# Kernel optimization log

Measured on AMD Instinct MI355X. Metric: run time of the kernel, lower is better.

## Reference

```python
import jax, jax.numpy as jnp
import numpy as np

N = 10000
E = 160000
NT = 4      # num_types
NB = 8      # bessel basis size
U = 32      # env_embed_multiplicity
R_MAX = 6.0
AVG_NEIGH = 16.0
POLY_P = 6.0


def _mlp(x, Ws):
    # nequip ScalarMLPFunction: no biases, forward-normalized weights, SiLU between layers
    n = len(Ws)
    for i, W in enumerate(Ws):
        x = x @ (W * (1.0 / jnp.sqrt(jnp.float32(W.shape[0]))))
        if i < n - 1:
            x = jax.nn.silu(x)
    return x


def _poly_cutoff(r, rc, p=POLY_P):
    x = r / rc
    out = (1.0 - ((p + 1.0) * (p + 2.0) / 2.0) * x ** p
           + p * (p + 2.0) * x ** (p + 1.0)
           - (p * (p + 1.0) / 2.0) * x ** (p + 2.0))
    return out * (x < 1.0)


def _weighted_channels(edge_attr, w):
    # MakeWeightedChannels: per-edge, per-channel weight for each irrep block
    # edge_attr: [E,4] = (0e | 1o), w: [E,U,2] -> out [E,U,4]
    wd = jnp.concatenate([w[:, :, 0:1], jnp.repeat(w[:, :, 1:2], 3, axis=-1)], axis=-1)
    return edge_attr[:, None, :] * wd


def _forward(edge_index, node_attrs, edge_attr, edge_embed, edge_length,
             W2b0, W2b1, W2b2, Wenv0, Wlat0, Wlat1, Wenv1, Wfin0, Wfin1,
             Wlin_s, Wlin_v, resnet_params):
    n_nodes = node_attrs.shape[0]
    n_edges = edge_attr.shape[0]
    center, neigh = edge_index[0], edge_index[1]
    cut = _poly_cutoff(edge_length, R_MAX)[:, None]           # [E,1], same per-layer cutoff
    env_norm = 1.0 / jnp.sqrt(AVG_NEIGH)
    sqrt3 = jnp.sqrt(3.0)
    c = jnp.exp(resnet_params)                                 # resnet update coefficients

    # ---- two-body latent (layer 0 latent)
    lat_in = jnp.concatenate([node_attrs[center], node_attrs[neigh], edge_embed], axis=-1)
    latents = _mlp(lat_in, [W2b0, W2b1, W2b2]) * cut           # [E,512]
    norm2 = c[0] ** 2
    latents = latents * (c[0] / jnp.sqrt(norm2))

    # env-embed MLP layer 0: feature weights + env weights
    w0 = _mlp(latents, [Wenv0])                                # [E,4U]
    w_feat = w0[:, :2 * U].reshape(n_edges, U, 2)
    w_env = w0[:, 2 * U:].reshape(n_edges, U, 2)
    features = _weighted_channels(edge_attr, w_feat)           # [E,U,4]

    def env_embed_edges(w_env):
        env_w = _weighted_channels(edge_attr, w_env)           # [E,U,4]
        env = jax.ops.segment_sum(env_w, center, num_segments=n_nodes) * env_norm
        return env[center]                                     # [E,U,4]

    # ---- layer 0 TP ('uuu', e3nn component norm): (0e+1o) x (0e+1o) -> [0e,0e,1o,1o]
    env_e = env_embed_edges(w_env)
    t0 = features[:, :, 0] * env_e[:, :, 0]
    t1 = jnp.sum(features[:, :, 1:] * env_e[:, :, 1:], axis=-1) / sqrt3
    v0 = features[:, :, 0:1] * env_e[:, :, 1:]
    v1 = features[:, :, 1:] * env_e[:, :, 0:1]
    scalars = jnp.concatenate([t0, t1], axis=-1)               # [E,2U]
    # e3nn Linear mixing full_out_irreps back to (0e+1o) x U
    alpha = 1.0 / jnp.sqrt(2.0 * U)
    y_s = (scalars @ Wlin_s) * alpha                           # [E,U]
    x_v = jnp.concatenate([v0, v1], axis=1)                    # [E,2U,3]
    y_v = jnp.einsum('ekd,ko->eod', x_v, Wlin_v) * alpha       # [E,U,3]
    features = jnp.concatenate([y_s[..., None], y_v], axis=-1)

    # latent resnet update
    new_lat = _mlp(jnp.concatenate([latents, scalars], axis=-1), [Wlat0, Wlat1]) * cut
    latents = (jnp.sqrt(norm2) * latents + c[1] * new_lat) / jnp.sqrt(norm2 + c[1] ** 2)
    norm2 = norm2 + c[1] ** 2

    w_env = _mlp(latents, [Wenv1]).reshape(n_edges, U, 2)

    # ---- layer 1 TP (last layer): only scalar outputs [0e,0e]
    env_e = env_embed_edges(w_env)
    t0 = features[:, :, 0] * env_e[:, :, 0]
    t1 = jnp.sum(features[:, :, 1:] * env_e[:, :, 1:], axis=-1) / sqrt3
    scalars = jnp.concatenate([t0, t1], axis=-1)               # [E,2U]
    # (the last-layer Linear output features are never used downstream -> skipped)

    # ---- final latent
    new_lat = _mlp(jnp.concatenate([latents, scalars], axis=-1), [Wfin0, Wfin1]) * cut
    latents = (jnp.sqrt(norm2) * latents + c[2] * new_lat) / jnp.sqrt(norm2 + c[2] ** 2)
    return latents                                             # [E,512] edge features


def setup_inputs() -> dict:
    key = jax.random.key(0)
    ks = jax.random.split(key, 20)
    edge_index = jax.random.randint(ks[0], (2, E), 0, N)
    node_types = jax.random.randint(ks[1], (N,), 0, NT)
    node_attrs = jax.nn.one_hot(node_types, NT, dtype=jnp.float32)
    edge_length = jax.random.uniform(ks[2], (E,), minval=0.5, maxval=R_MAX)
    vec = jax.random.normal(ks[3], (E, 3), dtype=jnp.float32)
    unit = vec / jnp.linalg.norm(vec, axis=-1, keepdims=True)
    # component-normalized real spherical harmonics: l=0 -> 1, l=1 -> sqrt(3)*unit
    edge_attr = jnp.concatenate([jnp.ones((E, 1), jnp.float32), jnp.sqrt(3.0) * unit], axis=-1)
    nb = jnp.arange(1, NB + 1, dtype=jnp.float32)
    edge_embed = (jnp.sqrt(2.0 / R_MAX)
                  * jnp.sin(nb[None, :] * jnp.pi * edge_length[:, None] / R_MAX)
                  / edge_length[:, None])
    w = lambda k, shp: jax.random.normal(k, shp, dtype=jnp.float32)
    return {
        'edge_index': edge_index, 'node_attrs': node_attrs, 'edge_attr': edge_attr,
        'edge_embed': edge_embed, 'edge_length': edge_length,
        'W2b0': w(ks[4], (2 * NT + NB, 128)), 'W2b1': w(ks[5], (128, 256)), 'W2b2': w(ks[6], (256, 512)),
        'Wenv0': w(ks[7], (512, 4 * U)),
        'Wlat0': w(ks[8], (512 + 2 * U, 512)), 'Wlat1': w(ks[9], (512, 512)),
        'Wenv1': w(ks[10], (512, 2 * U)),
        'Wfin0': w(ks[11], (512 + 2 * U, 512)), 'Wfin1': w(ks[12], (512, 512)),
        'Wlin_s': w(ks[13], (2 * U, U)), 'Wlin_v': w(ks[14], (2 * U, U)),
        'resnet_params': jnp.zeros((3,), jnp.float32),
    }


def reference(edge_index, node_attrs, edge_attr, edge_embed, edge_length,
              W2b0, W2b1, W2b2, Wenv0, Wlat0, Wlat1, Wenv1, Wfin0, Wfin1,
              Wlin_s, Wlin_v, resnet_params):
    return _forward(edge_index, node_attrs, edge_attr, edge_embed, edge_length,
                    W2b0, W2b1, W2b2, Wenv0, Wlat0, Wlat1, Wenv1, Wfin0, Wfin1,
                    Wlin_s, Wlin_v, resnet_params)
```

## Files before the change

kernel.cpp:

```cpp
#include <hip/hip_runtime.h>
#include <math.h>

#define E_EDGES 160000
#define N_NODES 10000

typedef __attribute__((ext_vector_type(8))) __bf16 bf16x8;
typedef __attribute__((ext_vector_type(4))) float f32x4;
typedef __attribute__((ext_vector_type(4))) unsigned int u32x4;

__device__ __forceinline__ unsigned short f2bf(float x) {
    unsigned u = __float_as_uint(x);
    u += 0x7fff + ((u >> 16) & 1);
    return (unsigned short)(u >> 16);
}
__device__ __forceinline__ float bf2f(unsigned short h) {
    return __uint_as_float(((unsigned)h) << 16);
}
__device__ __forceinline__ void gload16(const unsigned short* g, unsigned short* l) {
    __builtin_amdgcn_global_load_lds(
        (const __attribute__((address_space(1))) void*)g,
        (__attribute__((address_space(3))) void*)l, 16, 0, 0);
}

__global__ __launch_bounds__(256)
void prep_kernel(const int* __restrict__ ei, const float* __restrict__ na,
                 const float* __restrict__ embed, const float* __restrict__ elen,
                 float* __restrict__ cut, unsigned short* __restrict__ A16b,
                 int* __restrict__ deg)
{
    int e = blockIdx.x * blockDim.x + threadIdx.x;
    if (e >= E_EDGES) return;
    float r  = elen[e];
    float x  = r * (1.0f / 6.0f);
    float x2 = x * x;
    float x6 = x2 * x2 * x2;
    float c = 1.0f - 28.0f * x6 + 48.0f * x6 * x - 21.0f * x6 * x2;
    cut[e] = (x < 1.0f) ? c : 0.0f;
    int ctr = ei[e];
    int ngh = ei[E_EDGES + e];
    atomicAdd(&deg[ctr], 1);
    float4 ac = *(const float4*)(na + (size_t)ctr * 4);
    float4 an = *(const float4*)(na + (size_t)ngh * 4);
    float4 b0 = *(const float4*)(embed + (size_t)e * 8);
    float4 b1 = *(const float4*)(embed + (size_t)e * 8 + 4);
    unsigned short* o = A16b + (size_t)e * 32;
    o[0]  = f2bf(ac.x); o[1]  = f2bf(ac.y); o[2]  = f2bf(ac.z); o[3]  = f2bf(ac.w);
    o[4]  = f2bf(an.x); o[5]  = f2bf(an.y); o[6]  = f2bf(an.z); o[7]  = f2bf(an.w);
    o[8]  = f2bf(b0.x); o[9]  = f2bf(b0.y); o[10] = f2bf(b0.z); o[11] = f2bf(b0.w);
    o[12] = f2bf(b1.x); o[13] = f2bf(b1.y); o[14] = f2bf(b1.z); o[15] = f2bf(b1.w);
    #pragma unroll
    for (int i = 16; i < 32; ++i) o[i] = 0;
}

__global__ __launch_bounds__(256)
void wtrans_all(const float* __restrict__ w0, const float* __restrict__ w1,
                const float* __restrict__ w2, const float* __restrict__ w3,
                const float* __restrict__ w4, const float* __restrict__ w5,
                const float* __restrict__ w6, const float* __restrict__ w7,
                const float* __restrict__ w8, unsigned short* __restrict__ wbuf)
{
    int blk = blockIdx.x;
    const float* W; int K, N, Kpad, Npad; size_t dbase; int lstart; float sc;
    const float s16  = 0.25f;
    const float s128 = 0.088388347648318447f;
    const float s256 = 0.0625f;
    const float s512 = 0.044194173824159223f;
    const float s576 = 0.041666666666666664f;
    if      (blk <   16) { W=w0; K=16;  N=128; Kpad=32;  Npad=128; dbase=0;       lstart=0;    sc=s16;  }
    else if (blk <  144) { W=w1; K=128; N=256; Kpad=128; Npad=256; dbase=4096;    lstart=16;   sc=s128; }
    else if (blk <  656) { W=w2; K=256; N=512; Kpad=256; Npad=512; dbase=36864;   lstart=144;  sc=s256; }
    else if (blk <  912) { W=w3; K=512; N=128; Kpad=512; Npad=128; dbase=167936;  lstart=656;  sc=s512; }
    else if (blk < 2064) { W=w4; K=576; N=512; Kpad=576; Npad=512; dbase=233472;  lstart=912;  sc=s576; }
    else if (blk < 3088) { W=w5; K=512; N=512; Kpad=512; Npad=512; dbase=528384;  lstart=2064; sc=s512; }
    else if (blk < 3344) { W=w6; K=512; N=64;  Kpad=512; Npad=128; dbase=790528;  lstart=3088; sc=s512; }
    else if (blk < 4496) { W=w7; K=576; N=512; Kpad=576; Npad=512; dbase=856064;  lstart=3344; sc=s576; }
    else                 { W=w8; K=512; N=512; Kpad=512; Npad=512; dbase=1150976; lstart=4496; sc=s512; }
    int local = (blk - lstart) * 256 + threadIdx.x;
    int n = local % Npad, k = local / Npad;
    if (k >= Kpad) return;
    float v = (k < K && n < N) ? W[(size_t)k * N + n] * sc : 0.0f;
    wbuf[dbase + (size_t)n * Kpad + k] = f2bf(v);
}

__global__ __launch_bounds__(1024)
void scan_kernel(const int* __restrict__ deg, int* __restrict__ offs)
{
    __shared__ int part[1024];
    int t = threadIdx.x;
    int base = t * 10;
    int loc[10];
    int s = 0;
    #pragma unroll
    for (int i = 0; i < 10; ++i) {
        int idx = base + i;
        int d = (idx < N_NODES) ? deg[idx] : 0;
        loc[i] = s; s += d;
    }
    part[t] = s;
    __syncthreads();
    for (int o = 1; o < 1024; o <<= 1) {
        int v = (t >= o) ? part[t - o] : 0;
        __syncthreads();
        part[t] += v;
        __syncthreads();
    }
    int excl = (t > 0) ? part[t - 1] : 0;
    #pragma unroll
    for (int i = 0; i < 10; ++i) {
        int idx = base + i;
        if (idx < N_NODES) offs[idx] = excl + loc[i];
    }
    if (t == 1023) offs[N_NODES] = part[1023];
}

__global__ __launch_bounds__(256)
void fill_kernel(const int* __restrict__ ei, const int* __restrict__ offs,
                 int* __restrict__ cnt, int* __restrict__ elist)
{
    int e = blockIdx.x * blockDim.x + threadIdx.x;
    if (e >= E_EDGES) return;
    int c = ei[e];
    int pos = offs[c] + atomicAdd(&cnt[c], 1);
    elist[pos] = e;
}

__global__ __launch_bounds__(256)
void sortseg_kernel(const int* __restrict__ offs, int* __restrict__ elist)
{
    int node = blockIdx.x * 4 + (threadIdx.x >> 6);
    int l = threadIdx.x & 63;
    if (node >= N_NODES) return;
    int b = offs[node], en = offs[node + 1];
    int deg = en - b;
    if (deg <= 1) return;
    if (deg <= 64) {
        int v = (l < deg) ? elist[b + l] : 0x7fffffff;
        #pragma unroll
        for (int k = 2; k <= 64; k <<= 1) {
            #pragma unroll
            for (int j = k >> 1; j > 0; j >>= 1) {
                int o = __shfl_xor(v, j);
                bool dirUp = ((l & k) == 0);
                bool lower = ((l & j) == 0);
                int mn = v < o ? v : o;
                int mx = v < o ? o : v;
                v = (dirUp == lower) ? mn : mx;
            }
        }
        if (l < deg) elist[b + l] = v;
    } else if (l == 0) {
        for (int i = b + 1; i < en; ++i) {
            int v = elist[i];
            int j = i - 1;
            while (j >= b && elist[j] > v) { elist[j + 1] = elist[j]; --j; }
            elist[j + 1] = v;
        }
    }
}

__global__ __launch_bounds__(256)
void envgather_kernel(const unsigned short* __restrict__ Wb, int wstride, int woff,
                      const float* __restrict__ ea, const int* __restrict__ offs,
                      const int* __restrict__ elist, float* __restrict__ env)
{
    int n = blockIdx.x * 2 + (threadIdx.x >> 7);
    int t = threadIdx.x & 127;
    if (n >= N_NODES) return;
    int u = t >> 2, comp = t & 3;
    int widx = woff + u * 2 + (comp ? 1 : 0);
    int beg = offs[n], end = offs[n + 1];
    float acc = 0.0f;
    for (int i = beg; i < end; ++i) {
        int e = elist[i];
        float w = bf2f(Wb[(size_t)e * wstride + widx]);
        float a = ea[(size_t)e * 4 + comp];
        acc += a * w;
    }
    env[(size_t)n * 128 + t] = acc * 0.25f;
}

template<int EPIL, bool CONCAT>
__global__ __launch_bounds__(256)
void gemm_bf16(const unsigned short* __restrict__ A1, const unsigned short* __restrict__ A2,
               int KA1, int K, const unsigned short* __restrict__ Bt,
               int nx, int ldc, int Nstore,
               float* __restrict__ Cf, unsigned short* __restrict__ Cb,
               const float* __restrict__ cut, const float* __restrict__ rp)
{
    __shared__ __align__(16) unsigned short SB[3][2][128 * 32];
    const int tid  = threadIdx.x;
    const int lane = tid & 63;
    const int wid  = tid >> 6;
    const int wr   = wid >> 1, wc = wid & 1;
    const int nwg = gridDim.x;
    const int fid = blockIdx.x;
    const int q = nwg >> 3, r = nwg & 7;
    const int xcd = fid & 7, j = fid >> 3;
    const int L = ((xcd < r) ? xcd * (q + 1) : r * (q + 1) + (xcd - r) * q) + j;
    const int bn = (L % nx) * 128;
    const int bm = (L / nx) * 128;

    const int l15 = lane & 15;
    const int l4r = lane >> 2;
    const int sk8 = (((lane & 3) ^ ((lane >> 3) & 3)) << 3);
    const int rk8 = ((((lane >> 4) ^ ((l15 >> 1) & 3)) & 3) << 3);
    const int KA2 = K - KA1;
    const int T   = K >> 5;

    f32x4 acc[4][4] = {};

    auto stage = [&](int t, int b) {
        int k0 = t << 5;
        #pragma unroll
        for (int i = 0; i < 2; ++i) {
            int ch  = (wid << 1) + i;
            int row = (ch << 4) + l4r;
            const unsigned short* gp;
            if (!CONCAT || k0 < KA1)
                gp = A1 + (size_t)(bm + row) * KA1 + k0 + sk8;
            else
                gp = A2 + (size_t)(bm + row) * KA2 + (k0 - KA1) + sk8;
            gload16(gp, &SB[b][0][ch << 9]);
            const unsigned short* gpb = Bt + (size_t)(bn + row) * K + k0 + sk8;
            gload16(gpb, &SB[b][1][ch << 9]);
        }
    };

    stage(0, 0);
    if (T >= 2) stage(1, 1);

    for (int t = 0; t < T; ++t) {
        if (t < T - 1) asm volatile("s_waitcnt vmcnt(4)" ::: "memory");
        else           asm volatile("s_waitcnt vmcnt(0)" ::: "memory");
        __builtin_amdgcn_s_barrier();
        __builtin_amdgcn_sched_barrier(0);

        if (t + 2 < T) stage(t + 2, (t + 2) % 3);

        const unsigned short* As = &SB[t % 3][0][0];
        const unsigned short* Bs = &SB[t % 3][1][0];
        bf16x8 af[4], bfr[4];
        #pragma unroll
        for (int m = 0; m < 4; ++m)
            af[m] = __builtin_bit_cast(bf16x8, *(const u32x4*)&As[(wr * 64 + m * 16 + l15) * 32 + rk8]);
        #pragma unroll
        for (int n = 0; n < 4; ++n)
            bfr[n] = __builtin_bit_cast(bf16x8, *(const u32x4*)&Bs[(wc * 64 + n * 16 + l15) * 32 + rk8]);

        __builtin_amdgcn_s_setprio(1);
        #pragma unroll
        for (int m = 0; m < 4; ++m)
            #pragma unroll
            for (int n = 0; n < 4; ++n)
                acc[m][n] = __builtin_amdgcn_mfma_f32_16x16x32_bf16(af[m], bfr[n], acc[m][n], 0, 0, 0);
        __builtin_amdgcn_s_setprio(0);

        asm volatile("s_waitcnt lgkmcnt(0)" ::: "memory");
        __builtin_amdgcn_sched_barrier(0);
    }

    #pragma unroll
    for (int m = 0; m < 4; ++m) {
        int rbase = bm + wr * 64 + m * 16 + ((lane >> 4) << 2);
        #pragma unroll
        for (int n = 0; n < 4; ++n) {
            int col = bn + wc * 64 + n * 16 + l15;
            if (col < Nstore) {
                #pragma unroll
                for (int rr = 0; rr < 4; ++rr) {
                    int row = rbase + rr;
                    float v = acc[m][n][rr];
                    size_t off2 = (size_t)row * ldc + col;
                    if (EPIL == 0) {
                        Cb[off2] = f2bf(v);
                    } else if (EPIL == 1) {
                        v = v / (1.0f + __expf(-v));
                        Cb[off2] = f2bf(v);
                    } else if (EPIL == 2) {
                        v *= cut[row];
                        Cb[off2] = f2bf(v);
                    }
                }
            }
        }
    }
}

template<int EPIL2>
__global__ __launch_bounds__(512)
void fused_mlp(const unsigned short* __restrict__ A1,
               const unsigned short* __restrict__ A2,
               const unsigned short* __restrict__ W1t,
               const unsigned short* __restrict__ W2t,
               float* __restrict__ Cf, unsigned short* __restrict__ Cb,
               const float* __restrict__ cut, const float* __restrict__ rp)
{
    __shared__ __align__(16) unsigned short Hl[128 * 512];
    __shared__ __align__(16) unsigned short SA[3][128 * 32];
    const int tid  = threadIdx.x;
    const int lane = tid & 63;
    const int wid  = tid >> 6;
    const int l15  = lane & 15;
    const int l4r  = lane >> 2;
    const int lk8  = (lane >> 4) << 3;
    const int sk8  = (((lane & 3) ^ ((lane >> 3) & 3)) << 3);
    const int rk8  = ((((lane >> 4) ^ ((l15 >> 1) & 3)) & 3) << 3);
    const int bm   = blockIdx.x * 128;
    const int hcol0 = wid * 64;
    const int ocol0 = wid * 64;

    auto stage = [&](int t, int b) {
        int k0 = t << 5;
        int row = (wid << 4) + l4r;
        const unsigned short* gp;
        if (k0 < 512) gp = A1 + (size_t)(bm + row) * 512 + k0 + sk8;
        else          gp = A2 + (size_t)(bm + row) * 64 + (k0 - 512) + sk8;
        gload16(gp, &SA[b][wid << 9]);
    };

    f32x4 acc1[8][4] = {};
    stage(0, 0);
    stage(1, 1);

    for (int t = 0; t < 18; ++t) {
        __builtin_amdgcn_sched_barrier(0);
        if (t < 17) asm volatile("s_waitcnt vmcnt(1)" ::: "memory");
        else        asm volatile("s_waitcnt vmcnt(0)" ::: "memory");
        __builtin_amdgcn_s_barrier();
        __builtin_amdgcn_sched_barrier(0);

        const unsigned short* As = &SA[t % 3][0];
        int k0 = t << 5;
        bf16x8 af[8], wf[4];
        #pragma unroll
        for (int mi = 0; mi < 8; ++mi)
            af[mi] = __builtin_bit_cast(bf16x8, *(const u32x4*)&As[(mi * 16 + l15) * 32 + rk8]);
        #pragma unroll
        for (int ni = 0; ni < 4; ++ni) {
            int hc = hcol0 + ni * 16 + l15;
            wf[ni] = __builtin_bit_cast(bf16x8, *(const u32x4*)(W1t + (size_t)hc * 576 + k0 + lk8));
        }
        __builtin_amdgcn_sched_barrier(0);
        if (t + 2 < 18) stage(t + 2, (t + 2) % 3);
        __builtin_amdgcn_sched_barrier(0);
        asm volatile("s_waitcnt lgkmcnt(0)" ::: "memory");
        __builtin_amdgcn_sched_barrier(0);

        __builtin_amdgcn_s_setprio(1);
        #pragma unroll
        for (int mi = 0; mi < 8; ++mi)
            #pragma unroll
            for (int ni = 0; ni < 4; ++ni)
                acc1[mi][ni] = __builtin_amdgcn_mfma_f32_16x16x32_bf16(af[mi], wf[ni], acc1[mi][ni], 0, 0, 0);
        __builtin_amdgcn_s_setprio(0);
    }

    #pragma unroll
    for (int mi = 0; mi < 8; ++mi)
        #pragma unroll
        for (int ni = 0; ni < 4; ++ni)
            #pragma unroll
            for (int rr = 0; rr < 4; ++rr) {
                int er = mi * 16 + ((lane >> 4) << 2) + rr;
                int hc = hcol0 + ni * 16 + l15;
                float v = acc1[mi][ni][rr];
                v = v / (1.0f + __expf(-v));
                int slotp = (hc >> 3) ^ (er & 7);
                Hl[er * 512 + slotp * 8 + (hc & 7)] = f2bf(v);
            }
    asm volatile("s_waitcnt lgkmcnt(0)" ::: "memory");
    __builtin_amdgcn_s_barrier();
    __builtin_amdgcn_sched_barrier(0);

    f32x4 acc2[8][4] = {};
    #pragma unroll 1
    for (int kt = 0; kt < 16; ++kt) {
        bf16x8 hf[8], w2f[4];
        #pragma unroll
        for (int fa = 0; fa < 8; ++fa) {
            int er = fa * 16 + l15;
            int slotp = (kt * 4 + (lane >> 4)) ^ (er & 7);
            hf[fa] = __builtin_bit_cast(bf16x8, *(const u32x4*)&Hl[er * 512 + slotp * 8]);
        }
        #pragma unroll
        for (int fb = 0; fb < 4; ++fb) {
            int oc = ocol0 + fb * 16 + l15;
            w2f[fb] = __builtin_bit_cast(bf16x8, *(const u32x4*)(W2t + (size_t)oc * 512 + kt * 32 + lk8));
        }
        __builtin_amdgcn_s_setprio(1);
        #pragma unroll
        for (int fa = 0; fa < 8; ++fa)
            #pragma unroll
            for (int fb = 0; fb < 4; ++fb)
                acc2[fa][fb] = __builtin_amdgcn_mfma_f32_16x16x32_bf16(hf[fa], w2f[fb], acc2[fa][fb], 0, 0, 0);
        __builtin_amdgcn_s_setprio(0);
    }

    float c0 = __expf(rp[0]), c1 = __expf(rp[1]), c2 = __expf(rp[2]);
    #pragma unroll
    for (int fa = 0; fa < 8; ++fa) {
        int rbase = bm + fa * 16 + ((lane >> 4) << 2);
        #pragma unroll
        for (int fb = 0; fb < 4; ++fb) {
            int col = ocol0 + fb * 16 + l15;
            #pragma unroll
            for (int rr = 0; rr < 4; ++rr) {
                int row = rbase + rr;
                float v = acc2[fa][fb][rr];
                size_t off2 = (size_t)row * 512 + col;
                if (EPIL2 == 3) {
                    float old = bf2f(Cb[off2]);
                    v = (c0 * old + c1 * v * cut[row]) * rsqrtf(c0 * c0 + c1 * c1);
                    Cb[off2] = f2bf(v);
                } else {
                    float old = bf2f(Cb[off2]);
                    float n2 = c0 * c0 + c1 * c1;
                    v = (sqrtf(n2) * old + c2 * v * cut[row]) * rsqrtf(n2 + c2 * c2);
                    Cf[off2] = v;
                }
            }
        }
    }
}

__global__ __launch_bounds__(256)
void tp0_kernel(const unsigned short* __restrict__ W0b, const float* __restrict__ ea,
                const float* __restrict__ env, const int* __restrict__ ei,
                const float* __restrict__ Ws, const float* __restrict__ Wv,
                unsigned short* __restrict__ scalb, unsigned short* __restrict__ feat2b)
{
    __shared__ float sc[8][64];
    __shared__ float xv[8][64][3];
    __shared__ float Wsl[2048];
    __shared__ float Wvl[2048];
    int tid = threadIdx.x;
    const float alpha = 0.125f;
    #pragma unroll
    for (int i = 0; i < 8; ++i) {
        Wsl[tid + i * 256] = Ws[tid + i * 256] * alpha;
        Wvl[tid + i * 256] = Wv[tid + i * 256] * alpha;
    }
    int le = tid >> 5;
    int u  = tid & 31;
    int e  = blockIdx.x * 8 + le;
    int c  = ei[e];
    float4 a = *(const float4*)(ea + (size_t)e * 4);
    const float* ep = env + (size_t)c * 128 + u * 4;
    float e0 = ep[0], e1 = ep[1], e2 = ep[2], e3 = ep[3];
    float wf0 = bf2f(W0b[(size_t)e * 128 + u * 2]);
    float wf1 = bf2f(W0b[(size_t)e * 128 + u * 2 + 1]);
    float f0 = a.x * wf0;
    float f1 = a.y * wf1, f2 = a.z * wf1, f3 = a.w * wf1;
    const float rs3 = 0.57735026918962576f;
    float t0 = f0 * e0;
    float t1 = (f1 * e1 + f2 * e2 + f3 * e3) * rs3;
    scalb[(size_t)e * 64 + u]      = f2bf(t0);
    scalb[(size_t)e * 64 + 32 + u] = f2bf(t1);
    sc[le][u]      = t0;
    sc[le][32 + u] = t1;
    xv[le][u][0] = f0 * e1; xv[le][u][1] = f0 * e2; xv[le][u][2] = f0 * e3;
    xv[le][32 + u][0] = f1 * e0; xv[le][32 + u][1] = f2 * e0; xv[le][32 + u][2] = f3 * e0;
    __syncthreads();
    float ys = 0.0f, yv0 = 0.0f, yv1 = 0.0f, yv2 = 0.0f;
    #pragma unroll 8
    for (int k = 0; k < 64; ++k) {
        float ws = Wsl[k * 32 + u];
        float wv = Wvl[k * 32 + u];
        ys  = fmaf(sc[le][k], ws, ys);
        yv0 = fmaf(xv[le][k][0], wv, yv0);
        yv1 = fmaf(xv[le][k][1], wv, yv1);
        yv2 = fmaf(xv[le][k][2], wv, yv2);
    }
    ushort4 ov;
    ov.x = f2bf(ys);
    ov.y = f2bf(yv0);
    ov.z = f2bf(yv1);
    ov.w = f2bf(yv2);
    *(ushort4*)(feat2b + (size_t)e * 128 + u * 4) = ov;
}

__global__ __launch_bounds__(256)
void tp1_kernel(const unsigned short* __restrict__ feat2b, const float* __restrict__ env,
                const int* __restrict__ ei, unsigned short* __restrict__ scalb)
{
    int idx = blockIdx.x * blockDim.x + threadIdx.x;
    if (idx >= E_EDGES * 32) return;
    int e = idx >> 5, u = idx & 31;
    int c = ei[e];
    const float* ep = env + (size_t)c * 128 + u * 4;
    ushort4 f4 = *(const ushort4*)(feat2b + (size_t)e * 128 + u * 4);
    float fx = bf2f(f4.x), fy = bf2f(f4.y), fz = bf2f(f4.z), fw = bf2f(f4.w);
    const float rs3 = 0.57735026918962576f;
    float t0 = fx * ep[0];
    float t1 = (fy * ep[1] + fz * ep[2] + fw * ep[3]) * rs3;
    scalb[(size_t)e * 64 + u]      = f2bf(t0);
    scalb[(size_t)e * 64 + 32 + u] = f2bf(t1);
}

extern "C" void kernel_launch(void* const* d_in, const int* in_sizes, int n_in,
                              void* d_out, int out_size, void* d_ws, size_t ws_size,
                              hipStream_t stream)
{
    const int*   ei     = (const int*)d_in[0];
    const float* na     = (const float*)d_in[1];
    const float* ea     = (const float*)d_in[2];
    const float* embed  = (const float*)d_in[3];
    const float* elen   = (const float*)d_in[4];
    const float* W2b0   = (const float*)d_in[5];
    const float* W2b1   = (const float*)d_in[6];
    const float* W2b2   = (const float*)d_in[7];
    const float* Wenv0  = (const float*)d_in[8];
    const float* Wlat0  = (const float*)d_in[9];
    const float* Wlat1  = (const float*)d_in[10];
    const float* Wenv1  = (const float*)d_in[11];
    const float* Wfin0  = (const float*)d_in[12];
    const float* Wfin1  = (const float*)d_in[13];
    const float* Wlin_s = (const float*)d_in[14];
    const float* Wlin_v = (const float*)d_in[15];
    const float* rp     = (const float*)d_in[16];

    float* L = (float*)d_out;
    const size_t E = E_EDGES;

    char* ws = (char*)d_ws;
    size_t off = 0;
    auto alloc = [&](size_t b) { void* p = ws + off; off += (b + 255) & ~(size_t)255; return p; };
    float*          cutb   = (float*)alloc(E * 4);
    unsigned short* wbuf   = (unsigned short*)alloc((size_t)1413120 * 2);
    float*          envb   = (float*)alloc((size_t)N_NODES * 128 * 4);
    unsigned short* scalb  = (unsigned short*)alloc(E * 64 * 2);
    unsigned short* feat2b = (unsigned short*)alloc(E * 128 * 2);
    unsigned short* Lb     = (unsigned short*)alloc(E * 512 * 2);
    int*            degcnt = (int*)alloc((size_t)2 * N_NODES * 4);
    int*            offs   = (int*)alloc((N_NODES + 1) * 4);
    int*            elist  = (int*)alloc(E * 4);
    unsigned short* A16b   = (unsigned short*)alloc(E * 32 * 2);
    unsigned short* H1b    = (unsigned short*)alloc(E * 128 * 2);
    unsigned short* H2b    = (unsigned short*)alloc(E * 256 * 2);
    unsigned short* R1b    = (unsigned short*)alloc(E * 128 * 2);
    unsigned short* WE1b   = (unsigned short*)alloc(E * 64 * 2);
    int* deg = degcnt;
    int* cnt = degcnt + N_NODES;

    unsigned short* W2b0t  = wbuf;
    unsigned short* W2b1t  = wbuf + 4096;
    unsigned short* W2b2t  = wbuf + 36864;
    unsigned short* Wenv0t = wbuf + 167936;
    unsigned short* Wlat0t = wbuf + 233472;
    unsigned short* Wlat1t = wbuf + 528384;
    unsigned short* Wenv1t = wbuf + 790528;
    unsigned short* Wfin0t = wbuf + 856064;
    unsigned short* Wfin1t = wbuf + 1150976;
    wtrans_all<<<5520, 256, 0, stream>>>(W2b0, W2b1, W2b2, Wenv0, Wlat0, Wlat1,
                                         Wenv1, Wfin0, Wfin1, wbuf);

    hipMemsetAsync(degcnt, 0, (size_t)2 * N_NODES * 4, stream);
    prep_kernel<<<E_EDGES / 256, 256, 0, stream>>>(ei, na, embed, elen, cutb, A16b, deg);
    scan_kernel<<<1, 1024, 0, stream>>>(deg, offs);
    fill_kernel<<<E_EDGES / 256, 256, 0, stream>>>(ei, offs, cnt, elist);
    sortseg_kernel<<<N_NODES / 4, 256, 0, stream>>>(offs, elist);

    gemm_bf16<1, false><<<1250, 256, 0, stream>>>(A16b, nullptr, 32, 32, W2b0t, 1, 128, 128, nullptr, H1b, nullptr, nullptr);
    gemm_bf16<1, false><<<2500, 256, 0, stream>>>(H1b, nullptr, 128, 128, W2b1t, 2, 256, 256, nullptr, H2b, nullptr, nullptr);
    gemm_bf16<2, false><<<5000, 256, 0, stream>>>(H2b, nullptr, 256, 256, W2b2t, 4, 512, 512, nullptr, Lb, cutb, nullptr);

    gemm_bf16<0, false><<<1250, 256, 0, stream>>>(Lb, nullptr, 512, 512, Wenv0t, 1, 128, 128, nullptr, R1b, nullptr, nullptr);

    envgather_kernel<<<N_NODES / 2, 256, 0, stream>>>(R1b, 128, 64, ea, offs, elist, envb);
    tp0_kernel<<<E_EDGES / 8, 256, 0, stream>>>(R1b, ea, envb, ei, Wlin_s, Wlin_v, scalb, feat2b);

    fused_mlp<3><<<1250, 512, 0, stream>>>(Lb, scalb, Wlat0t, Wlat1t, nullptr, Lb, cutb, rp);

    gemm_bf16<0, false><<<1250, 256, 0, stream>>>(Lb, nullptr, 512, 512, Wenv1t, 1, 64, 64, nullptr, WE1b, nullptr, nullptr);

    envgather_kernel<<<N_NODES / 2, 256, 0, stream>>>(WE1b, 64, 0, ea, offs, elist, envb);
    tp1_kernel<<<E_EDGES * 32 / 256, 256, 0, stream>>>(feat2b, envb, ei, scalb);

    fused_mlp<4><<<1250, 512, 0, stream>>>(Lb, scalb, Wfin0t, Wfin1t, L, Lb, cutb, rp);
}
```

Measured before the change: 1.183 ms.

## Fuse two-body MLP into one kernel and halve fused_mlp row tile

Replaces the three separate two-body MLP GEMMs with a single mlp2b kernel that keeps the hidden activations (128 and 256 wide) in LDS per 64-edge tile, removing the global write and read of the H1/H2 intermediates. The fused_mlp kernels also drop from 128-row to 64-row tiles, halving LDS use and accumulator registers and doubling the grid, which should allow more resident blocks. The cost is that weights are re-read per smaller tile, and the mlp2b weight fragments are loaded directly from global memory without staging.

```diff
diff --git a/kernel.cpp b/kernel.cpp
--- a/kernel.cpp
+++ b/kernel.cpp
@@ -15,6 +15,9 @@
 }
 __device__ __forceinline__ float bf2f(unsigned short h) {
     return __uint_as_float(((unsigned)h) << 16);
+}
+__device__ __forceinline__ float siluf(float v) {
+    return v / (1.0f + __expf(-v));
 }
 __device__ __forceinline__ void gload16(const unsigned short* g, unsigned short* l) {
     __builtin_amdgcn_global_load_lds(
@@ -179,13 +182,12 @@
     env[(size_t)n * 128 + t] = acc * 0.25f;
 }
 
-template<int EPIL, bool CONCAT>
-__global__ __launch_bounds__(256)
-void gemm_bf16(const unsigned short* __restrict__ A1, const unsigned short* __restrict__ A2,
-               int KA1, int K, const unsigned short* __restrict__ Bt,
+template<int EPIL>
+__global__ __launch_bounds__(256)
+void gemm_bf16(const unsigned short* __restrict__ A1,
+               int K, const unsigned short* __restrict__ Bt,
                int nx, int ldc, int Nstore,
-               float* __restrict__ Cf, unsigned short* __restrict__ Cb,
-               const float* __restrict__ cut, const float* __restrict__ rp)
+               unsigned short* __restrict__ Cb)
 {
     __shared__ __align__(16) unsigned short SB[3][2][128 * 32];
     const int tid  = threadIdx.x;
@@ -204,7 +206,6 @@
     const int l4r = lane >> 2;
     const int sk8 = (((lane & 3) ^ ((lane >> 3) & 3)) << 3);
     const int rk8 = ((((lane >> 4) ^ ((l15 >> 1) & 3)) & 3) << 3);
-    const int KA2 = K - KA1;
     const int T   = K >> 5;
 
     f32x4 acc[4][4] = {};
@@ -215,14 +216,8 @@
         for (int i = 0; i < 2; ++i) {
             int ch  = (wid << 1) + i;
             int row = (ch << 4) + l4r;
-            const unsigned short* gp;
-            if (!CONCAT || k0 < KA1)
-                gp = A1 + (size_t)(bm + row) * KA1 + k0 + sk8;
-            else
-                gp = A2 + (size_t)(bm + row) * KA2 + (k0 - KA1) + sk8;
-            gload16(gp, &SB[b][0][ch << 9]);
-            const unsigned short* gpb = Bt + (size_t)(bn + row) * K + k0 + sk8;
-            gload16(gpb, &SB[b][1][ch << 9]);
+            gload16(A1 + (size_t)(bm + row) * K + k0 + sk8, &SB[b][0][ch << 9]);
+            gload16(Bt + (size_t)(bn + row) * K + k0 + sk8, &SB[b][1][ch << 9]);
         }
     };
 
@@ -269,18 +264,133 @@
                 #pragma unroll
                 for (int rr = 0; rr < 4; ++rr) {
                     int row = rbase + rr;
-                    float v = acc[m][n][rr];
-                    size_t off2 = (size_t)row * ldc + col;
-                    if (EPIL == 0) {
-                        Cb[off2] = f2bf(v);
-                    } else if (EPIL == 1) {
-                        v = v / (1.0f + __expf(-v));
-                        Cb[off2] = f2bf(v);
-                    } else if (EPIL == 2) {
-                        v *= cut[row];
-                        Cb[off2] = f2bf(v);
-                    }
+                    Cb[(size_t)row * ldc + col] = f2bf(acc[m][n][rr]);
                 }
+            }
+        }
+    }
+}
+
+__global__ __launch_bounds__(512)
+void mlp2b(const unsigned short* __restrict__ A16b,
+           const unsigned short* __restrict__ W0t,
+           const unsigned short* __restrict__ W1t,
+           const unsigned short* __restrict__ W2t,
+           const float* __restrict__ cut, unsigned short* __restrict__ Lb)
+{
+    __shared__ __align__(16) unsigned short SA[64 * 32];
+    __shared__ __align__(16) unsigned short H1[64 * 128];
+    __shared__ __align__(16) unsigned short H2[64 * 256];
+    const int tid  = threadIdx.x;
+    const int lane = tid & 63;
+    const int wid  = tid >> 6;
+    const int l15  = lane & 15;
+    const int l4r  = lane >> 2;
+    const int lk8  = (lane >> 4) << 3;
+    const int sk8  = (((lane & 3) ^ ((lane >> 3) & 3)) << 3);
+    const int rk8  = ((((lane >> 4) ^ ((l15 >> 1) & 3)) & 3) << 3);
+    const int bm   = blockIdx.x * 64;
+    const int hrow4 = (lane >> 4) << 2;
+
+    if (wid < 4) {
+        int row = (wid << 4) + l4r;
+        gload16(A16b + (size_t)(bm + row) * 32 + sk8, &SA[wid << 9]);
+    }
+    asm volatile("s_waitcnt vmcnt(0)" ::: "memory");
+    __builtin_amdgcn_s_barrier();
+    __builtin_amdgcn_sched_barrier(0);
+
+    {
+        int hc = wid * 16 + l15;
+        bf16x8 wf = __builtin_bit_cast(bf16x8, *(const u32x4*)(W0t + (size_t)hc * 32 + lk8));
+        #pragma unroll
+        for (int mi = 0; mi < 4; ++mi) {
+            bf16x8 af = __builtin_bit_cast(bf16x8, *(const u32x4*)&SA[(mi * 16 + l15) * 32 + rk8]);
+            f32x4 a = {};
+            a = __builtin_amdgcn_mfma_f32_16x16x32_bf16(af, wf, a, 0, 0, 0);
+            #pragma unroll
+            for (int rr = 0; rr < 4; ++rr) {
+                int er = mi * 16 + hrow4 + rr;
+                H1[er * 128 + (((hc >> 3) ^ (er & 7)) << 3) + (hc & 7)] = f2bf(siluf(a[rr]));
+            }
+        }
+    }
+    asm volatile("s_waitcnt lgkmcnt(0)" ::: "memory");
+    __builtin_amdgcn_s_barrier();
+    __builtin_amdgcn_sched_barrier(0);
+
+    {
+        f32x4 acc[4][2] = {};
+        #pragma unroll
+        for (int kt = 0; kt < 4; ++kt) {
+            bf16x8 hf[4], wf[2];
+            #pragma unroll
+            for (int fa = 0; fa < 4; ++fa) {
+                int er = fa * 16 + l15;
+                int slotp = (kt * 4 + (lane >> 4)) ^ (er & 7);
+                hf[fa] = __builtin_bit_cast(bf16x8, *(const u32x4*)&H1[er * 128 + slotp * 8]);
+            }
+            #pragma unroll
+            for (int fb = 0; fb < 2; ++fb) {
+                int hc = wid * 32 + fb * 16 + l15;
+                wf[fb] = __builtin_bit_cast(bf16x8, *(const u32x4*)(W1t + (size_t)hc * 128 + kt * 32 + lk8));
+            }
+            #pragma unroll
+            for (int fa = 0; fa < 4; ++fa)
+                #pragma unroll
+                for (int fb = 0; fb < 2; ++fb)
+                    acc[fa][fb] = __builtin_amdgcn_mfma_f32_16x16x32_bf16(hf[fa], wf[fb], acc[fa][fb], 0, 0, 0);
+        }
+        asm volatile("s_waitcnt lgkmcnt(0)" ::: "memory");
+        __builtin_amdgcn_s_barrier();
+        #pragma unroll
+        for (int fa = 0; fa < 4; ++fa)
+            #pragma unroll
+            for (int fb = 0; fb < 2; ++fb)
+                #pragma unroll
+                for (int rr = 0; rr < 4; ++rr) {
+                    int er = fa * 16 + hrow4 + rr;
+                    int hc = wid * 32 + fb * 16 + l15;
+                    H2[er * 256 + (((hc >> 3) ^ (er & 7)) << 3) + (hc & 7)] = f2bf(siluf(acc[fa][fb][rr]));
+                }
+    }
+    asm volatile("s_waitcnt lgkmcnt(0)" ::: "memory");
+    __builtin_amdgcn_s_barrier();
+    __builtin_amdgcn_sched_barrier(0);
+
+    f32x4 acc[4][4] = {};
+    #pragma unroll 1
+    for (int kt = 0; kt < 8; ++kt) {
+        bf16x8 hf[4], wf[4];
+        #pragma unroll
+        for (int fa = 0; fa < 4; ++fa) {
+            int er = fa * 16 + l15;
+            int slotp = (kt * 4 + (lane >> 4)) ^ (er & 7);
+            hf[fa] = __builtin_bit_cast(bf16x8, *(const u32x4*)&H2[er * 256 + slotp * 8]);
+        }
+        #pragma unroll
+        for (int fb = 0; fb < 4; ++fb) {
+            int oc = wid * 64 + fb * 16 + l15;
+            wf[fb] = __builtin_bit_cast(bf16x8, *(const u32x4*)(W2t + (size_t)oc * 256 + kt * 32 + lk8));
+        }
+        __builtin_amdgcn_s_setprio(1);
+        #pragma unroll
+        for (int fa = 0; fa < 4; ++fa)
+            #pragma unroll
+            for (int fb = 0; fb < 4; ++fb)
+                acc[fa][fb] = __builtin_amdgcn_mfma_f32_16x16x32_bf16(hf[fa], wf[fb], acc[fa][fb], 0, 0, 0);
+        __builtin_amdgcn_s_setprio(0);
+    }
+    #pragma unroll
+    for (int fa = 0; fa < 4; ++fa) {
+        int rbase = bm + fa * 16 + hrow4;
+        #pragma unroll
+        for (int fb = 0; fb < 4; ++fb) {
+            int col = wid * 64 + fb * 16 + l15;
+            #pragma unroll
+            for (int rr = 0; rr < 4; ++rr) {
+                int row = rbase + rr;
+                Lb[(size_t)row * 512 + col] = f2bf(acc[fa][fb][rr] * cut[row]);
             }
         }
     }
@@ -295,8 +405,8 @@
                float* __restrict__ Cf, unsigned short* __restrict__ Cb,
                const float* __restrict__ cut, const float* __restrict__ rp)
 {
-    __shared__ __align__(16) unsigned short Hl[128 * 512];
-    __shared__ __align__(16) unsigned short SA[3][128 * 32];
+    __shared__ __align__(16) unsigned short Hl[64 * 512];
+    __shared__ __align__(16) unsigned short SA[3][64 * 32];
     const int tid  = threadIdx.x;
     const int lane = tid & 63;
     const int wid  = tid >> 6;
@@ -305,20 +415,22 @@
     const int lk8  = (lane >> 4) << 3;
     const int sk8  = (((lane & 3) ^ ((lane >> 3) & 3)) << 3);
     const int rk8  = ((((lane >> 4) ^ ((l15 >> 1) & 3)) & 3) << 3);
-    const int bm   = blockIdx.x * 128;
-    const int hcol0 = wid * 64;
-    const int ocol0 = wid * 64;
+    const int bm   = blockIdx.x * 64;
+    const int col0 = wid * 64;
+    const int hrow4 = (lane >> 4) << 2;
 
     auto stage = [&](int t, int b) {
-        int k0 = t << 5;
-        int row = (wid << 4) + l4r;
-        const unsigned short* gp;
-        if (k0 < 512) gp = A1 + (size_t)(bm + row) * 512 + k0 + sk8;
-        else          gp = A2 + (size_t)(bm + row) * 64 + (k0 - 512) + sk8;
-        gload16(gp, &SA[b][wid << 9]);
+        if (wid < 4) {
+            int k0 = t << 5;
+            int row = (wid << 4) + l4r;
+            const unsigned short* gp;
+            if (k0 < 512) gp = A1 + (size_t)(bm + row) * 512 + k0 + sk8;
+            else          gp = A2 + (size_t)(bm + row) * 64 + (k0 - 512) + sk8;
+            gload16(gp, &SA[b][wid << 9]);
+        }
     };
 
-    f32x4 acc1[8][4] = {};
+    f32x4 acc1[4][4] = {};
     stage(0, 0);
     stage(1, 1);
 
@@ -331,13 +443,13 @@
 
         const unsigned short* As = &SA[t % 3][0];
         int k0 = t << 5;
-        bf16x8 af[8], wf[4];
-        #pragma unroll
-        for (int mi = 0; mi < 8; ++mi)
+        bf16x8 af[4], wf[4];
+        #pragma unroll
+        for (int mi = 0; mi < 4; ++mi)
             af[mi] = __builtin_bit_cast(bf16x8, *(const u32x4*)&As[(mi * 16 + l15) * 32 + rk8]);
         #pragma unroll
         for (int ni = 0; ni < 4; ++ni) {
-            int hc = hcol0 + ni * 16 + l15;
+            int hc = col0 + ni * 16 + l15;
             wf[ni] = __builtin_bit_cast(bf16x8, *(const u32x4*)(W1t + (size_t)hc * 576 + k0 + lk8));
         }
         __builtin_amdgcn_sched_barrier(0);
@@ -348,7 +460,7 @@
 
         __builtin_amdgcn_s_setprio(1);
         #pragma unroll
-        for (int mi = 0; mi < 8; ++mi)
+        for (int mi = 0; mi < 4; ++mi)
             #pragma unroll
             for (int ni = 0; ni < 4; ++ni)
                 acc1[mi][ni] = __builtin_amdgcn_mfma_f32_16x16x32_bf16(af[mi], wf[ni], acc1[mi][ni], 0, 0, 0);
@@ -356,40 +468,37 @@
     }
 
     #pragma unroll
-    for (int mi = 0; mi < 8; ++mi)
+    for (int mi = 0; mi < 4; ++mi)
         #pragma unroll
         for (int ni = 0; ni < 4; ++ni)
             #pragma unroll
             for (int rr = 0; rr < 4; ++rr) {
-                int er = mi * 16 + ((lane >> 4) << 2) + rr;
-                int hc = hcol0 + ni * 16 + l15;
-                float v = acc1[mi][ni][rr];
-                v = v / (1.0f + __expf(-v));
-                int slotp = (hc >> 3) ^ (er & 7);
-                Hl[er * 512 + slotp * 8 + (hc & 7)] = f2bf(v);
+                int er = mi * 16 + hrow4 + rr;
+                int hc = col0 + ni * 16 + l15;
+                Hl[er * 512 + (((hc >> 3) ^ (er & 7)) << 3) + (hc & 7)] = f2bf(siluf(acc1[mi][ni][rr]));
             }
     asm volatile("s_waitcnt lgkmcnt(0)" ::: "memory");
     __builtin_amdgcn_s_barrier();
     __builtin_amdgcn_sched_barrier(0);
 
-    f32x4 acc2[8][4] = {};
+    f32x4 acc2[4][4] = {};
     #pragma unroll 1
     for (int kt = 0; kt < 16; ++kt) {
-        bf16x8 hf[8], w2f[4];
-        #pragma unroll
-        for (int fa = 0; fa < 8; ++fa) {
+        bf16x8 hf[4], w2f[4];
+        #pragma unroll
+        for (int fa = 0; fa < 4; ++fa) {
             int er = fa * 16 + l15;
             int slotp = (kt * 4 + (lane >> 4)) ^ (er & 7);
             hf[fa] = __builtin_bit_cast(bf16x8, *(const u32x4*)&Hl[er * 512 + slotp * 8]);
         }
         #pragma unroll
         for (int fb = 0; fb < 4; ++fb) {
-            int oc = ocol0 + fb * 16 + l15;
+            int oc = col0 + fb * 16 + l15;
             w2f[fb] = __builtin_bit_cast(bf16x8, *(const u32x4*)(W2t + (size_t)oc * 512 + kt * 32 + lk8));
         }
         __builtin_amdgcn_s_setprio(1);
         #pragma unroll
-        for (int fa = 0; fa < 8; ++fa)
+        for (int fa = 0; fa < 4; ++fa)
             #pragma unroll
             for (int fb = 0; fb < 4; ++fb)
                 acc2[fa][fb] = __builtin_amdgcn_mfma_f32_16x16x32_bf16(hf[fa], w2f[fb], acc2[fa][fb], 0, 0, 0);
@@ -398,11 +507,11 @@
 
     float c0 = __expf(rp[0]), c1 = __expf(rp[1]), c2 = __expf(rp[2]);
     #pragma unroll
-    for (int fa = 0; fa < 8; ++fa) {
-        int rbase = bm + fa * 16 + ((lane >> 4) << 2);
+    for (int fa = 0; fa < 4; ++fa) {
+        int rbase = bm + fa * 16 + hrow4;
         #pragma unroll
         for (int fb = 0; fb < 4; ++fb) {
-            int col = ocol0 + fb * 16 + l15;
+            int col = col0 + fb * 16 + l15;
             #pragma unroll
             for (int rr = 0; rr < 4; ++rr) {
                 int row = rbase + rr;
@@ -535,8 +644,6 @@
     int*            offs   = (int*)alloc((N_NODES + 1) * 4);
     int*            elist  = (int*)alloc(E * 4);
     unsigned short* A16b   = (unsigned short*)alloc(E * 32 * 2);
-    unsigned short* H1b    = (unsigned short*)alloc(E * 128 * 2);
-    unsigned short* H2b    = (unsigned short*)alloc(E * 256 * 2);
     unsigned short* R1b    = (unsigned short*)alloc(E * 128 * 2);
     unsigned short* WE1b   = (unsigned short*)alloc(E * 64 * 2);
     int* deg = degcnt;
@@ -560,21 +667,19 @@
     fill_kernel<<<E_EDGES / 256, 256, 0, stream>>>(ei, offs, cnt, elist);
     sortseg_kernel<<<N_NODES / 4, 256, 0, stream>>>(offs, elist);
 
-    gemm_bf16<1, false><<<1250, 256, 0, stream>>>(A16b, nullptr, 32, 32, W2b0t, 1, 128, 128, nullptr, H1b, nullptr, nullptr);
-    gemm_bf16<1, false><<<2500, 256, 0, stream>>>(H1b, nullptr, 128, 128, W2b1t, 2, 256, 256, nullptr, H2b, nullptr, nullptr);
-    gemm_bf16<2, false><<<5000, 256, 0, stream>>>(H2b, nullptr, 256, 256, W2b2t, 4, 512, 512, nullptr, Lb, cutb, nullptr);
-
-    gemm_bf16<0, false><<<1250, 256, 0, stream>>>(Lb, nullptr, 512, 512, Wenv0t, 1, 128, 128, nullptr, R1b, nullptr, nullptr);
+    mlp2b<<<2500, 512, 0, stream>>>(A16b, W2b0t, W2b1t, W2b2t, cutb, Lb);
+
+    gemm_bf16<0><<<1250, 256, 0, stream>>>(Lb, 512, Wenv0t, 1, 128, 128, R1b);
 
     envgather_kernel<<<N_NODES / 2, 256, 0, stream>>>(R1b, 128, 64, ea, offs, elist, envb);
     tp0_kernel<<<E_EDGES / 8, 256, 0, stream>>>(R1b, ea, envb, ei, Wlin_s, Wlin_v, scalb, feat2b);
 
-    fused_mlp<3><<<1250, 512, 0, stream>>>(Lb, scalb, Wlat0t, Wlat1t, nullptr, Lb, cutb, rp);
-
-    gemm_bf16<0, false><<<1250, 256, 0, stream>>>(Lb, nullptr, 512, 512, Wenv1t, 1, 64, 64, nullptr, WE1b, nullptr, nullptr);
+    fused_mlp<3><<<2500, 512, 0, stream>>>(Lb, scalb, Wlat0t, Wlat1t, nullptr, Lb, cutb, rp);
+
+    gemm_bf16<0><<<1250, 256, 0, stream>>>(Lb, 512, Wenv1t, 1, 64, 64, WE1b);
 
     envgather_kernel<<<N_NODES / 2, 256, 0, stream>>>(WE1b, 64, 0, ea, offs, elist, envb);
     tp1_kernel<<<E_EDGES * 32 / 256, 256, 0, stream>>>(feat2b, envb, ei, scalb);
 
-    fused_mlp<4><<<1250, 512, 0, stream>>>(Lb, scalb, Wfin0t, Wfin1t, L, Lb, cutb, rp);
-}
+    fused_mlp<4><<<2500, 512, 0, stream>>>(Lb, scalb, Wfin0t, Wfin1t, L, Lb, cutb, rp);
+}
```

Result: slower. 1.372 ms (+15.9%).
